# Performance work log

Hardware: AMD Instinct MI355X
Metric: run time of the kernel (lower is better)

The kernel has to match this reference:

```python
import jax, jax.numpy as jnp
import numpy as np

VOCAB, EMBED, HIDDEN = 50000, 256, 512
B, SEQ = 64, 200


def setup_inputs() -> dict:
    key = jax.random.key(0)
    ks = jax.random.split(key, 16)
    h2 = 2 * HIDDEN
    inp = {
        "input_idx": jax.random.randint(ks[0], (B,), 0, VOCAB),
        "encoded": jax.random.normal(ks[1], (B, SEQ, h2), jnp.float32),
        "encoded_idx": jax.random.randint(ks[2], (B, SEQ), 0, VOCAB),
        "prev_state": jax.random.normal(ks[3], (B, HIDDEN), jnp.float32),
        "weighted": jax.random.normal(ks[4], (B, 1, h2), jnp.float32),
        "order": 1,
        # learned parameters
        "embed_table": jax.random.normal(ks[5], (VOCAB, EMBED), jnp.float32) * 0.02,
        "w_ih": jax.random.normal(ks[6], (3 * HIDDEN, EMBED + h2), jnp.float32) * 0.02,
        "w_hh": jax.random.normal(ks[7], (3 * HIDDEN, HIDDEN), jnp.float32) * 0.02,
        "b_ih": jax.random.normal(ks[8], (3 * HIDDEN,), jnp.float32) * 0.02,
        "b_hh": jax.random.normal(ks[9], (3 * HIDDEN,), jnp.float32) * 0.02,
        "wo_w": jax.random.normal(ks[10], (VOCAB, HIDDEN), jnp.float32) * 0.02,
        "wo_b": jax.random.normal(ks[11], (VOCAB,), jnp.float32) * 0.02,
        "wc_w": jax.random.normal(ks[12], (HIDDEN, h2), jnp.float32) * 0.02,
        "wc_b": jax.random.normal(ks[13], (HIDDEN,), jnp.float32) * 0.02,
    }
    return inp


def _gru_step(x, h, w_ih, w_hh, b_ih, b_hh):
    # torch GRU gate ordering: reset, update, new
    gx = x @ w_ih.T + b_ih            # [b, 3h]
    gh = h @ w_hh.T + b_hh            # [b, 3h]
    xr, xz, xn = jnp.split(gx, 3, axis=-1)
    hr, hz, hn = jnp.split(gh, 3, axis=-1)
    r = jax.nn.sigmoid(xr + hr)
    z = jax.nn.sigmoid(xz + hz)
    n = jnp.tanh(xn + r * hn)
    return (1.0 - z) * n + z * h


def reference(input_idx, encoded, encoded_idx, prev_state, weighted, order,
              embed_table, w_ih, w_hh, b_ih, b_hh, wo_w, wo_b, wc_w, wc_b):
    b, seq, _ = encoded.shape
    vocab = wo_w.shape[0]

    # GRU single step on [embed(input); weighted]
    x = jnp.concatenate([embed_table[input_idx], weighted[:, 0, :]], axis=-1)
    state = _gru_step(x, prev_state, w_ih, w_hh, b_ih, b_hh)  # [b, h]

    # generate score over vocab
    score_g = state @ wo_w.T + wo_b                           # [b, vocab]

    # copy score over source positions
    score_c = jnp.tanh(jnp.einsum('bsk,hk->bsh', encoded, wc_w) + wc_b)
    score_c = jnp.einsum('bsh,bh->bs', score_c, state)        # [b, seq]

    encoded_mask = (encoded_idx != 0).astype(score_c.dtype)
    idx_from_input = (encoded_idx == input_idx[:, None]).astype(score_c.dtype)
    score_c = score_c * encoded_mask * idx_from_input

    # joint softmax over [vocab + seq]
    probs = jax.nn.softmax(jnp.concatenate([score_g, score_c], axis=1), axis=1)
    prob_g = probs[:, :vocab]
    prob_c = probs[:, vocab:]                                 # [b, seq]

    # scatter copy probs into vocab space (equivalent to one-hot bmm)
    flat_idx = (jnp.arange(b)[:, None] * vocab + encoded_idx).reshape(-1)
    prob_c_to_g = jnp.zeros((b * vocab,), probs.dtype).at[flat_idx].add(
        prob_c.reshape(-1)).reshape(b, vocab)

    out = (prob_g + prob_c_to_g)[:, None, :]                  # [b, 1, vocab]

    # selective-read attention, renormalized where sum > 0 (detached divisor)
    attn = prob_c * idx_from_input
    s = jax.lax.stop_gradient(jnp.sum(attn, axis=1, keepdims=True))
    attn = jnp.where(s > 0.0, attn / jnp.where(s > 0.0, s, 1.0), attn)
    weighted_new = jnp.einsum('bs,bsk->bk', attn, encoded)[:, None, :]  # [b,1,2h]

    return out, state, weighted_new
```

## Files before the change

kernel.cpp:

```cpp
#include <hip/hip_runtime.h>
#include <hip/hip_bf16.h>
#include <cstdint>
#include <cstddef>

#define VOCAB  50000
#define EMBED  256
#define HIDDEN 512
#define BATCH  64
#define SEQ    200
#define H2     1024
#define XDIM   1280
#define G3     1536
#define V4     (VOCAB/4)
#define NVB    782
#define NVBP   784
#define NFB    13

typedef __attribute__((ext_vector_type(8))) short short8;
typedef __attribute__((ext_vector_type(4))) float f32x4;

__device__ __forceinline__ short f2bf(float f) {
  uint32_t u = __builtin_bit_cast(uint32_t, f);
  uint32_t r = (u + 0x7fffu + ((u >> 16) & 1u)) >> 16;
  return (short)(r & 0xffffu);
}

__device__ __forceinline__ short8 pack8(float4 v0, float4 v1) {
  short8 fr;
  fr[0]=f2bf(v0.x); fr[1]=f2bf(v0.y); fr[2]=f2bf(v0.z); fr[3]=f2bf(v0.w);
  fr[4]=f2bf(v1.x); fr[5]=f2bf(v1.y); fr[6]=f2bf(v1.z); fr[7]=f2bf(v1.w);
  return fr;
}

__launch_bounds__(256)
__global__ void gru_gemm(const int* __restrict__ idx, const float* __restrict__ embed,
                         const float* __restrict__ weighted, const float* __restrict__ h0,
                         const float* __restrict__ w_ih, const float* __restrict__ w_hh,
                         float* __restrict__ gxp, float* __restrict__ ghp) {
  __shared__ __align__(16) short As[4 * 64 * 8];
  const int tid  = threadIdx.x;
  const int wave = tid >> 6, lane = tid & 63;
  const int l15  = lane & 15, lk = lane >> 4;
  const int slice = blockIdx.y;
  const bool isX  = slice < 8;
  const float* B  = isX ? w_ih : w_hh;
  const int ldb   = isX ? XDIM : HIDDEN;
  const int kbeg  = isX ? slice * 160 : (slice - 8) * 128;
  const int kend  = kbeg + (isX ? 160 : 128);
  float* C = isX ? (gxp + (size_t)slice * BATCH * G3)
                 : (ghp + (size_t)(slice - 8) * BATCH * G3);
  const int ncol = blockIdx.x * 64 + wave * 16;

  f32x4 acc0 = {0,0,0,0}, acc1 = {0,0,0,0}, acc2 = {0,0,0,0}, acc3 = {0,0,0,0};

  const int sl  = tid & 63;
  const int sm  = (tid >> 6) * 16 + (sl & 15);
  const int skb = (sl >> 4) * 8;

  const int nrow = ncol + l15;
  const float* Bbase = B + (size_t)nrow * ldb + lk * 8;

  for (int kc = kbeg; kc < kend; kc += 32) {
    {
      const float4* ap;
      if (isX) {
        int col = kc + skb;
        if (col < EMBED) ap = reinterpret_cast<const float4*>(embed + (size_t)idx[sm] * EMBED + col);
        else             ap = reinterpret_cast<const float4*>(weighted + (size_t)sm * H2 + (col - EMBED));
      } else {
        ap = reinterpret_cast<const float4*>(h0 + (size_t)sm * HIDDEN + kc + skb);
      }
      *reinterpret_cast<short8*>(&As[tid * 8]) = pack8(ap[0], ap[1]);
    }
    __syncthreads();
    short8 bf;
    {
      const float4* bp = reinterpret_cast<const float4*>(Bbase + kc);
      bf = pack8(bp[0], bp[1]);
    }
    short8 a0 = *reinterpret_cast<const short8*>(&As[(0*64 + lane)*8]);
    short8 a1 = *reinterpret_cast<const short8*>(&As[(1*64 + lane)*8]);
    short8 a2 = *reinterpret_cast<const short8*>(&As[(2*64 + lane)*8]);
    short8 a3 = *reinterpret_cast<const short8*>(&As[(3*64 + lane)*8]);
    acc0 = __builtin_amdgcn_mfma_f32_16x16x32_bf16(a0, bf, acc0, 0, 0, 0);
    acc1 = __builtin_amdgcn_mfma_f32_16x16x32_bf16(a1, bf, acc1, 0, 0, 0);
    acc2 = __builtin_amdgcn_mfma_f32_16x16x32_bf16(a2, bf, acc2, 0, 0, 0);
    acc3 = __builtin_amdgcn_mfma_f32_16x16x32_bf16(a3, bf, acc3, 0, 0, 0);
    __syncthreads();
  }

  const int n = ncol + l15;
  #pragma unroll
  for (int r = 0; r < 4; ++r) {
    C[(size_t)(0*16 + lk*4 + r) * G3 + n] = acc0[r];
    C[(size_t)(1*16 + lk*4 + r) * G3 + n] = acc1[r];
    C[(size_t)(2*16 + lk*4 + r) * G3 + n] = acc2[r];
    C[(size_t)(3*16 + lk*4 + r) * G3 + n] = acc3[r];
  }
}

__launch_bounds__(256)
__global__ void gru_gates(const float* __restrict__ gxp, const float* __restrict__ ghp,
                          const float* __restrict__ b_ih, const float* __restrict__ b_hh,
                          const float* __restrict__ h0, float* __restrict__ out_state,
                          unsigned short* __restrict__ stateF) {
  int i = blockIdx.x * 256 + threadIdx.x;
  int b = i >> 9, h = i & 511;
  float xr = b_ih[h], xz = b_ih[HIDDEN + h], xn = b_ih[2*HIDDEN + h];
  #pragma unroll
  for (int s = 0; s < 8; ++s) {
    const float* g = gxp + (size_t)s * BATCH * G3 + (size_t)b * G3;
    xr += g[h]; xz += g[HIDDEN + h]; xn += g[2*HIDDEN + h];
  }
  float hr = b_hh[h], hz = b_hh[HIDDEN + h], hn = b_hh[2*HIDDEN + h];
  #pragma unroll
  for (int s = 0; s < 4; ++s) {
    const float* g = ghp + (size_t)s * BATCH * G3 + (size_t)b * G3;
    hr += g[h]; hz += g[HIDDEN + h]; hn += g[2*HIDDEN + h];
  }
  float r = 1.f / (1.f + __expf(-(xr + hr)));
  float z = 1.f / (1.f + __expf(-(xz + hz)));
  float n = tanhf(xn + r * hn);
  float st = (1.f - z) * n + z * h0[(size_t)b*HIDDEN + h];
  out_state[(size_t)b*HIDDEN + h] = st;
  int fi = ((h >> 5) * 4 + (b >> 4)) * 512 + ((b & 15) + 16 * ((h >> 3) & 3)) * 8 + (h & 7);
  stateF[fi] = (unsigned short)f2bf(st);
}

__launch_bounds__(256)
__global__ void vocab_fused(const unsigned short* __restrict__ stateF,
                            const float* __restrict__ state,
                            const float* __restrict__ wo_w, const float* __restrict__ wo_b,
                            const int* __restrict__ eidx, const int* __restrict__ iidx,
                            const float* __restrict__ enc, const float* __restrict__ wc_w,
                            const float* __restrict__ wc_b,
                            float* __restrict__ E, float* __restrict__ escc,
                            float* __restrict__ Spart) {
  __shared__ float red[256];
  __shared__ float sval[SEQ];
  __shared__ int   act[SEQ];
  const int bid = blockIdx.x;
  const int tid = threadIdx.x;

  if (bid < BATCH) {
    const int b = bid;
    const int in0 = iidx[b];
    if (tid < SEQ) {
      int e = eidx[b*SEQ + tid];
      act[tid]  = (e != 0 && e == in0);
      sval[tid] = 0.f;
    }
    __syncthreads();
    for (int sq = 0; sq < SEQ; ++sq) {
      if (act[sq]) {
        const float4* er = reinterpret_cast<const float4*>(enc + (size_t)b*SEQ*H2 + (size_t)sq*H2);
        float part_sum = 0.f;
        for (int h = tid; h < HIDDEN; h += 256) {
          const float4* wr = reinterpret_cast<const float4*>(wc_w + (size_t)h*H2);
          float d = wc_b[h];
          for (int k = 0; k < H2/4; ++k) {
            float4 a = er[k], w = wr[k];
            d += a.x*w.x + a.y*w.y + a.z*w.z + a.w*w.w;
          }
          part_sum += tanhf(d) * state[(size_t)b*HIDDEN + h];
        }
        red[tid] = part_sum;
        __syncthreads();
        for (int off = 128; off > 0; off >>= 1) {
          if (tid < off) red[tid] += red[tid + off];
          __syncthreads();
        }
        if (tid == 0) sval[sq] = red[0];
        __syncthreads();
      }
    }
    __syncthreads();
    float ex = 0.f;
    if (tid < SEQ) {
      ex = __expf(sval[tid]);
      escc[b*SEQ + tid] = ex;
    }
    red[tid] = ex;
    __syncthreads();
    for (int off = 128; off > 0; off >>= 1) {
      if (tid < off) red[tid] += red[tid + off];
      __syncthreads();
    }
    if (tid == 0) Spart[(size_t)b * NVBP + NVB] = red[0];
    return;
  }

  const int vb   = bid - BATCH;
  const int wave = tid >> 6, lane = tid & 63;
  const int l15  = lane & 15, lk = lane >> 4;
  const int ncol = vb * 64 + wave * 16;
  int nrow = ncol + l15; if (nrow > VOCAB - 1) nrow = VOCAB - 1;
  const float*  Bb = wo_w + (size_t)nrow * HIDDEN + lk * 8;
  const short8* Af = reinterpret_cast<const short8*>(stateF);

  f32x4 acc0 = {0,0,0,0}, acc1 = {0,0,0,0}, acc2 = {0,0,0,0}, acc3 = {0,0,0,0};
  #pragma unroll 4
  for (int c = 0; c < 16; ++c) {
    const float4* bp = reinterpret_cast<const float4*>(Bb + c*32);
    float4 b0 = bp[0], b1 = bp[1];
    short8 a0 = Af[(c*4 + 0)*64 + lane];
    short8 a1 = Af[(c*4 + 1)*64 + lane];
    short8 a2 = Af[(c*4 + 2)*64 + lane];
    short8 a3 = Af[(c*4 + 3)*64 + lane];
    short8 bf = pack8(b0, b1);
    acc0 = __builtin_amdgcn_mfma_f32_16x16x32_bf16(a0, bf, acc0, 0, 0, 0);
    acc1 = __builtin_amdgcn_mfma_f32_16x16x32_bf16(a1, bf, acc1, 0, 0, 0);
    acc2 = __builtin_amdgcn_mfma_f32_16x16x32_bf16(a2, bf, acc2, 0, 0, 0);
    acc3 = __builtin_amdgcn_mfma_f32_16x16x32_bf16(a3, bf, acc3, 0, 0, 0);
  }

  const int n = ncol + l15;
  const bool valid = n < VOCAB;
  const float bv = valid ? wo_b[n] : 0.f;
  f32x4 accs[4] = {acc0, acc1, acc2, acc3};
  #pragma unroll
  for (int a = 0; a < 4; ++a) {
    #pragma unroll
    for (int r = 0; r < 4; ++r) {
      float ev = valid ? __expf(accs[a][r] + bv) : 0.f;
      if (valid) E[(size_t)(a*16 + lk*4 + r) * VOCAB + n] = ev;
      float v = ev;
      v += __shfl_xor(v, 1); v += __shfl_xor(v, 2);
      v += __shfl_xor(v, 4); v += __shfl_xor(v, 8);
      if (l15 == 0) red[wave*64 + a*16 + lk*4 + r] = v;
    }
  }
  __syncthreads();
  if (tid < 64)
    Spart[(size_t)tid * NVBP + vb] =
        red[0*64+tid] + red[1*64+tid] + red[2*64+tid] + red[3*64+tid];
}

__launch_bounds__(256)
__global__ void finalize_fused(const int* __restrict__ eidx, const int* __restrict__ iidx,
                               const float* __restrict__ escc, const float* __restrict__ Spart,
                               const float* __restrict__ enc,
                               float* __restrict__ out0, float* __restrict__ wnew) {
  const int bid = blockIdx.x;
  const int tid = threadIdx.x;

  if (bid < BATCH) {
    __shared__ float attn_sh[SEQ];
    __shared__ float fnorm_sh;
    const int b = bid;
    const int in0 = iidx[b];
    if (tid < SEQ) {
      int e = eidx[b*SEQ + tid];
      attn_sh[tid] = (e == in0) ? escc[b*SEQ + tid] : 0.f;
    }
    __syncthreads();
    if (tid == 0) {
      float s = 0.f;
      for (int i = 0; i < SEQ; ++i) s += attn_sh[i];
      fnorm_sh = (s > 0.f) ? 1.f / s : 1.f;
    }
    __syncthreads();
    const float f = fnorm_sh;
    float a0 = 0, a1 = 0, a2 = 0, a3 = 0;
    const float4* ep = reinterpret_cast<const float4*>(enc + (size_t)b*SEQ*H2);
    for (int s = 0; s < SEQ; ++s) {
      float a = attn_sh[s];
      if (a != 0.f) {
        a *= f;
        float4 v = ep[(size_t)s*(H2/4) + tid];
        a0 += a*v.x; a1 += a*v.y; a2 += a*v.z; a3 += a*v.w;
      }
    }
    float4 o = {a0, a1, a2, a3};
    reinterpret_cast<float4*>(wnew + (size_t)b*H2)[tid] = o;
    return;
  }

  __shared__ int   me[SEQ];
  __shared__ float mp[SEQ];
  __shared__ float sred[256];
  __shared__ int   cnt;
  const int q = bid - BATCH;
  const int b = q / NFB, c = q % NFB;
  if (tid == 0) cnt = 0;
  float ps = 0.f;
  for (int i = tid; i < NVB + 1; i += 256) ps += Spart[(size_t)b * NVBP + i];
  sred[tid] = ps;
  __syncthreads();
  if (tid < SEQ) {
    int e = eidx[b*SEQ + tid];
    if ((unsigned)(e - c*4096) < 4096u) {
      int j = atomicAdd(&cnt, 1);
      me[j] = e; mp[j] = escc[b*SEQ + tid];
    }
  }
  for (int off = 128; off > 0; off >>= 1) {
    __syncthreads();
    if (tid < off) sred[tid] += sred[tid + off];
  }
  __syncthreads();
  const float inv = 1.f / sred[0];
  const int ncnt = cnt;
  #pragma unroll
  for (int t = 0; t < 4; ++t) {
    const int i4 = c * 1024 + t * 256 + tid;
    if (i4 < V4) {
      float4 v = reinterpret_cast<const float4*>(out0 + (size_t)b*VOCAB)[i4];
      float4 o;
      o.x = v.x * inv; o.y = v.y * inv; o.z = v.z * inv; o.w = v.w * inv;
      const int base = i4 * 4;
      for (int j = 0; j < ncnt; ++j) {
        unsigned d = (unsigned)(me[j] - base);
        if (d < 4u) (&o.x)[d] += mp[j] * inv;
      }
      reinterpret_cast<float4*>(out0 + (size_t)b*VOCAB)[i4] = o;
    }
  }
}

extern "C" void kernel_launch(void* const* d_in, const int* in_sizes, int n_in,
                              void* d_out, int out_size, void* d_ws, size_t ws_size,
                              hipStream_t stream) {
  (void)in_sizes; (void)n_in; (void)out_size; (void)ws_size;
  const int*   input_idx  = (const int*)d_in[0];
  const float* encoded    = (const float*)d_in[1];
  const int*   enc_idx    = (const int*)d_in[2];
  const float* prev_state = (const float*)d_in[3];
  const float* weighted   = (const float*)d_in[4];
  const float* embed      = (const float*)d_in[6];
  const float* w_ih       = (const float*)d_in[7];
  const float* w_hh       = (const float*)d_in[8];
  const float* b_ih       = (const float*)d_in[9];
  const float* b_hh       = (const float*)d_in[10];
  const float* wo_w       = (const float*)d_in[11];
  const float* wo_b       = (const float*)d_in[12];
  const float* wc_w       = (const float*)d_in[13];
  const float* wc_b       = (const float*)d_in[14];

  float* out0      = (float*)d_out;
  float* out_state = out0 + (size_t)BATCH * VOCAB;
  float* out_wnew  = out_state + BATCH * HIDDEN;

  float* ws    = (float*)d_ws;
  float* gxp   = ws;
  float* ghp   = ws + (size_t)8 * BATCH * G3;
  unsigned short* stateF = (unsigned short*)(ws + (size_t)12 * BATCH * G3);
  float* escc  = ws + (size_t)12 * BATCH * G3 + 16384;
  float* Spart = escc + BATCH * SEQ;

  gru_gemm<<<dim3(G3/64, 12), 256, 0, stream>>>(input_idx, embed, weighted, prev_state,
                                                w_ih, w_hh, gxp, ghp);
  gru_gates<<<(BATCH*HIDDEN)/256, 256, 0, stream>>>(gxp, ghp, b_ih, b_hh, prev_state,
                                                    out_state, stateF);
  vocab_fused<<<BATCH + NVB, 256, 0, stream>>>(stateF, out_state, wo_w, wo_b,
                                               enc_idx, input_idx, encoded, wc_w, wc_b,
                                               out0, escc, Spart);
  finalize_fused<<<BATCH + BATCH*NFB, 256, 0, stream>>>(enc_idx, input_idx, escc, Spart,
                                                        encoded, out0, out_wnew);
}
```

Measured before the change: 83.16 us.

## Fuse vocab GEMM and finalize into one cooperative kernel with grid syncs

Merges the vocab projection kernel and the finalize kernel into a single cooperative launch. The exp'd logits stay in registers across grid-wide barriers and are normalized and scattered in place, instead of being written to the output and re-read in a second pass. Each vocab block rescans all encoded indices to build its own copy-scatter list in shared memory. The MFMA loop is also software-pipelined with a one-step prefetch. In exchange it pays for two grid syncs, the redundant index scans, and a fixed MCAP limit on the scatter list.

```diff
diff --git a/kernel.cpp b/kernel.cpp
--- a/kernel.cpp
+++ b/kernel.cpp
@@ -1,7 +1,10 @@
 #include <hip/hip_runtime.h>
+#include <hip/hip_cooperative_groups.h>
 #include <hip/hip_bf16.h>
 #include <cstdint>
 #include <cstddef>
+
+namespace cg = cooperative_groups;
 
 #define VOCAB  50000
 #define EMBED  256
@@ -14,7 +17,7 @@
 #define V4     (VOCAB/4)
 #define NVB    782
 #define NVBP   784
-#define NFB    13
+#define MCAP   2048
 
 typedef __attribute__((ext_vector_type(8))) short short8;
 typedef __attribute__((ext_vector_type(4))) float f32x4;
@@ -127,18 +130,24 @@
   stateF[fi] = (unsigned short)f2bf(st);
 }
 
-__launch_bounds__(256)
-__global__ void vocab_fused(const unsigned short* __restrict__ stateF,
-                            const float* __restrict__ state,
-                            const float* __restrict__ wo_w, const float* __restrict__ wo_b,
-                            const int* __restrict__ eidx, const int* __restrict__ iidx,
-                            const float* __restrict__ enc, const float* __restrict__ wc_w,
-                            const float* __restrict__ wc_b,
-                            float* __restrict__ E, float* __restrict__ escc,
-                            float* __restrict__ Spart) {
+__launch_bounds__(256, 4)
+__global__ void vocab_coop(const unsigned short* __restrict__ stateF,
+                           const float* __restrict__ state,
+                           const float* __restrict__ wo_w, const float* __restrict__ wo_b,
+                           const int* __restrict__ eidx, const int* __restrict__ iidx,
+                           const float* __restrict__ enc, const float* __restrict__ wc_w,
+                           const float* __restrict__ wc_b,
+                           float* __restrict__ out0, float* __restrict__ wnew,
+                           float* __restrict__ escc, float* __restrict__ Spart,
+                           float* __restrict__ Svec) {
+  cg::grid_group grid = cg::this_grid();
   __shared__ float red[256];
   __shared__ float sval[SEQ];
   __shared__ int   act[SEQ];
+  __shared__ int   me[MCAP];
+  __shared__ float mprob[MCAP];
+  __shared__ float Ssh[BATCH];
+  __shared__ int   mcnt;
   const int bid = blockIdx.x;
   const int tid = threadIdx.x;
 
@@ -187,6 +196,45 @@
       __syncthreads();
     }
     if (tid == 0) Spart[(size_t)b * NVBP + NVB] = red[0];
+    __threadfence();
+    grid.sync();
+
+    float ps = 0.f;
+    for (int i = tid; i < NVB + 1; i += 256) ps += Spart[(size_t)b * NVBP + i];
+    red[tid] = ps;
+    __syncthreads();
+    for (int off = 128; off > 0; off >>= 1) {
+      if (tid < off) red[tid] += red[tid + off];
+      __syncthreads();
+    }
+    if (tid == 0) Svec[b] = red[0];
+
+    {
+      float attn = 0.f;
+      float fsum = 0.f;
+      if (tid == 0) {
+        float s = 0.f;
+        for (int i = 0; i < SEQ; ++i)
+          if (act[i]) s += __expf(sval[i]);
+        red[0] = (s > 0.f) ? 1.f / s : 1.f;
+      }
+      __syncthreads();
+      const float f = red[0];
+      (void)attn; (void)fsum;
+      float a0 = 0, a1 = 0, a2 = 0, a3 = 0;
+      const float4* ep = reinterpret_cast<const float4*>(enc + (size_t)b*SEQ*H2);
+      for (int s = 0; s < SEQ; ++s) {
+        if (act[s]) {
+          float a = __expf(sval[s]) * f;
+          float4 v = ep[(size_t)s*(H2/4) + tid];
+          a0 += a*v.x; a1 += a*v.y; a2 += a*v.z; a3 += a*v.w;
+        }
+      }
+      float4 o = {a0, a1, a2, a3};
+      reinterpret_cast<float4*>(wnew + (size_t)b*H2)[tid] = o;
+    }
+    __threadfence();
+    grid.sync();
     return;
   }
 
@@ -198,122 +246,119 @@
   const float*  Bb = wo_w + (size_t)nrow * HIDDEN + lk * 8;
   const short8* Af = reinterpret_cast<const short8*>(stateF);
 
+  if (tid == 0) mcnt = 0;
+
   f32x4 acc0 = {0,0,0,0}, acc1 = {0,0,0,0}, acc2 = {0,0,0,0}, acc3 = {0,0,0,0};
-  #pragma unroll 4
-  for (int c = 0; c < 16; ++c) {
-    const float4* bp = reinterpret_cast<const float4*>(Bb + c*32);
-    float4 b0 = bp[0], b1 = bp[1];
-    short8 a0 = Af[(c*4 + 0)*64 + lane];
-    short8 a1 = Af[(c*4 + 1)*64 + lane];
-    short8 a2 = Af[(c*4 + 2)*64 + lane];
-    short8 a3 = Af[(c*4 + 3)*64 + lane];
-    short8 bf = pack8(b0, b1);
-    acc0 = __builtin_amdgcn_mfma_f32_16x16x32_bf16(a0, bf, acc0, 0, 0, 0);
-    acc1 = __builtin_amdgcn_mfma_f32_16x16x32_bf16(a1, bf, acc1, 0, 0, 0);
-    acc2 = __builtin_amdgcn_mfma_f32_16x16x32_bf16(a2, bf, acc2, 0, 0, 0);
-    acc3 = __builtin_amdgcn_mfma_f32_16x16x32_bf16(a3, bf, acc3, 0, 0, 0);
+  {
+    const float4* bp0 = reinterpret_cast<const float4*>(Bb);
+    float4 b0 = bp0[0], b1 = bp0[1];
+    short8 a0 = Af[0*64 + lane], a1 = Af[1*64 + lane];
+    short8 a2 = Af[2*64 + lane], a3 = Af[3*64 + lane];
+    #pragma unroll
+    for (int c = 0; c < 16; ++c) {
+      float4 nb0, nb1; short8 n0, n1, n2, n3;
+      if (c < 15) {
+        const float4* bp = reinterpret_cast<const float4*>(Bb + (c+1)*32);
+        nb0 = bp[0]; nb1 = bp[1];
+        n0 = Af[((c+1)*4 + 0)*64 + lane];
+        n1 = Af[((c+1)*4 + 1)*64 + lane];
+        n2 = Af[((c+1)*4 + 2)*64 + lane];
+        n3 = Af[((c+1)*4 + 3)*64 + lane];
+      }
+      short8 bf = pack8(b0, b1);
+      acc0 = __builtin_amdgcn_mfma_f32_16x16x32_bf16(a0, bf, acc0, 0, 0, 0);
+      acc1 = __builtin_amdgcn_mfma_f32_16x16x32_bf16(a1, bf, acc1, 0, 0, 0);
+      acc2 = __builtin_amdgcn_mfma_f32_16x16x32_bf16(a2, bf, acc2, 0, 0, 0);
+      acc3 = __builtin_amdgcn_mfma_f32_16x16x32_bf16(a3, bf, acc3, 0, 0, 0);
+      if (c < 15) { b0 = nb0; b1 = nb1; a0 = n0; a1 = n1; a2 = n2; a3 = n3; }
+    }
   }
 
   const int n = ncol + l15;
   const bool valid = n < VOCAB;
   const float bv = valid ? wo_b[n] : 0.f;
-  f32x4 accs[4] = {acc0, acc1, acc2, acc3};
-  #pragma unroll
-  for (int a = 0; a < 4; ++a) {
-    #pragma unroll
-    for (int r = 0; r < 4; ++r) {
-      float ev = valid ? __expf(accs[a][r] + bv) : 0.f;
-      if (valid) E[(size_t)(a*16 + lk*4 + r) * VOCAB + n] = ev;
-      float v = ev;
-      v += __shfl_xor(v, 1); v += __shfl_xor(v, 2);
-      v += __shfl_xor(v, 4); v += __shfl_xor(v, 8);
-      if (l15 == 0) red[wave*64 + a*16 + lk*4 + r] = v;
+  #pragma unroll
+  for (int r = 0; r < 4; ++r) {
+    acc0[r] = valid ? __expf(acc0[r] + bv) : 0.f;
+    acc1[r] = valid ? __expf(acc1[r] + bv) : 0.f;
+    acc2[r] = valid ? __expf(acc2[r] + bv) : 0.f;
+    acc3[r] = valid ? __expf(acc3[r] + bv) : 0.f;
+  }
+  #pragma unroll
+  for (int r = 0; r < 4; ++r) {
+    float v0 = acc0[r], v1 = acc1[r], v2 = acc2[r], v3 = acc3[r];
+    v0 += __shfl_xor(v0,1); v0 += __shfl_xor(v0,2); v0 += __shfl_xor(v0,4); v0 += __shfl_xor(v0,8);
+    v1 += __shfl_xor(v1,1); v1 += __shfl_xor(v1,2); v1 += __shfl_xor(v1,4); v1 += __shfl_xor(v1,8);
+    v2 += __shfl_xor(v2,1); v2 += __shfl_xor(v2,2); v2 += __shfl_xor(v2,4); v2 += __shfl_xor(v2,8);
+    v3 += __shfl_xor(v3,1); v3 += __shfl_xor(v3,2); v3 += __shfl_xor(v3,4); v3 += __shfl_xor(v3,8);
+    if (l15 == 0) {
+      red[wave*64 + 0*16 + lk*4 + r] = v0;
+      red[wave*64 + 1*16 + lk*4 + r] = v1;
+      red[wave*64 + 2*16 + lk*4 + r] = v2;
+      red[wave*64 + 3*16 + lk*4 + r] = v3;
     }
   }
   __syncthreads();
   if (tid < 64)
     Spart[(size_t)tid * NVBP + vb] =
         red[0*64+tid] + red[1*64+tid] + red[2*64+tid] + red[3*64+tid];
-}
-
-__launch_bounds__(256)
-__global__ void finalize_fused(const int* __restrict__ eidx, const int* __restrict__ iidx,
-                               const float* __restrict__ escc, const float* __restrict__ Spart,
-                               const float* __restrict__ enc,
-                               float* __restrict__ out0, float* __restrict__ wnew) {
-  const int bid = blockIdx.x;
-  const int tid = threadIdx.x;
-
-  if (bid < BATCH) {
-    __shared__ float attn_sh[SEQ];
-    __shared__ float fnorm_sh;
-    const int b = bid;
-    const int in0 = iidx[b];
-    if (tid < SEQ) {
-      int e = eidx[b*SEQ + tid];
-      attn_sh[tid] = (e == in0) ? escc[b*SEQ + tid] : 0.f;
-    }
-    __syncthreads();
-    if (tid == 0) {
-      float s = 0.f;
-      for (int i = 0; i < SEQ; ++i) s += attn_sh[i];
-      fnorm_sh = (s > 0.f) ? 1.f / s : 1.f;
-    }
-    __syncthreads();
-    const float f = fnorm_sh;
-    float a0 = 0, a1 = 0, a2 = 0, a3 = 0;
-    const float4* ep = reinterpret_cast<const float4*>(enc + (size_t)b*SEQ*H2);
-    for (int s = 0; s < SEQ; ++s) {
-      float a = attn_sh[s];
-      if (a != 0.f) {
-        a *= f;
-        float4 v = ep[(size_t)s*(H2/4) + tid];
-        a0 += a*v.x; a1 += a*v.y; a2 += a*v.z; a3 += a*v.w;
-      }
-    }
-    float4 o = {a0, a1, a2, a3};
-    reinterpret_cast<float4*>(wnew + (size_t)b*H2)[tid] = o;
-    return;
-  }
-
-  __shared__ int   me[SEQ];
-  __shared__ float mp[SEQ];
-  __shared__ float sred[256];
-  __shared__ int   cnt;
-  const int q = bid - BATCH;
-  const int b = q / NFB, c = q % NFB;
-  if (tid == 0) cnt = 0;
-  float ps = 0.f;
-  for (int i = tid; i < NVB + 1; i += 256) ps += Spart[(size_t)b * NVBP + i];
-  sred[tid] = ps;
+
+  const int colLo = vb * 64;
+  for (int j = tid; j < BATCH*SEQ; j += 256) {
+    int e = eidx[j];
+    if ((unsigned)(e - colLo) < 64u) {
+      int k = atomicAdd(&mcnt, 1);
+      if (k < MCAP) me[k] = (j << 16) | e;
+    }
+  }
   __syncthreads();
-  if (tid < SEQ) {
-    int e = eidx[b*SEQ + tid];
-    if ((unsigned)(e - c*4096) < 4096u) {
-      int j = atomicAdd(&cnt, 1);
-      me[j] = e; mp[j] = escc[b*SEQ + tid];
-    }
-  }
-  for (int off = 128; off > 0; off >>= 1) {
-    __syncthreads();
-    if (tid < off) sred[tid] += sred[tid + off];
-  }
+  __threadfence();
+  grid.sync();
+  grid.sync();
+
+  if (tid < BATCH) Ssh[tid] = Svec[tid];
+  int nc = mcnt; if (nc > MCAP) nc = MCAP;
   __syncthreads();
-  const float inv = 1.f / sred[0];
-  const int ncnt = cnt;
-  #pragma unroll
-  for (int t = 0; t < 4; ++t) {
-    const int i4 = c * 1024 + t * 256 + tid;
-    if (i4 < V4) {
-      float4 v = reinterpret_cast<const float4*>(out0 + (size_t)b*VOCAB)[i4];
-      float4 o;
-      o.x = v.x * inv; o.y = v.y * inv; o.z = v.z * inv; o.w = v.w * inv;
-      const int base = i4 * 4;
-      for (int j = 0; j < ncnt; ++j) {
-        unsigned d = (unsigned)(me[j] - base);
-        if (d < 4u) (&o.x)[d] += mp[j] * inv;
-      }
-      reinterpret_cast<float4*>(out0 + (size_t)b*VOCAB)[i4] = o;
+  for (int k = tid; k < nc; k += 256) {
+    int j = me[k] >> 16;
+    int b = j / SEQ, s = j - b * SEQ;
+    mprob[k] = escc[b*SEQ + s] / Ssh[b];
+  }
+  __syncthreads();
+
+  #pragma unroll
+  for (int r = 0; r < 4; ++r) {
+    acc0[r] *= 1.f / Ssh[0*16 + lk*4 + r];
+    acc1[r] *= 1.f / Ssh[1*16 + lk*4 + r];
+    acc2[r] *= 1.f / Ssh[2*16 + lk*4 + r];
+    acc3[r] *= 1.f / Ssh[3*16 + lk*4 + r];
+  }
+
+  for (int k = 0; k < nc; ++k) {
+    const int pk = me[k];
+    const int e  = pk & 0xffff;
+    const int j  = pk >> 16;
+    const int b  = j / SEQ;
+    const bool laneHit = (((e - colLo) >> 4) == wave) && ((e & 15) == l15)
+                         && (((b >> 2) & 3) == lk);
+    const float add = laneHit ? mprob[k] : 0.f;
+    const int ba = b >> 4, br = b & 3;
+    #pragma unroll
+    for (int r = 0; r < 4; ++r) {
+      acc0[r] += (ba == 0 && br == r) ? add : 0.f;
+      acc1[r] += (ba == 1 && br == r) ? add : 0.f;
+      acc2[r] += (ba == 2 && br == r) ? add : 0.f;
+      acc3[r] += (ba == 3 && br == r) ? add : 0.f;
+    }
+  }
+
+  if (valid) {
+    #pragma unroll
+    for (int r = 0; r < 4; ++r) {
+      out0[(size_t)(0*16 + lk*4 + r) * VOCAB + n] = acc0[r];
+      out0[(size_t)(1*16 + lk*4 + r) * VOCAB + n] = acc1[r];
+      out0[(size_t)(2*16 + lk*4 + r) * VOCAB + n] = acc2[r];
+      out0[(size_t)(3*16 + lk*4 + r) * VOCAB + n] = acc3[r];
     }
   }
 }
@@ -347,14 +392,20 @@
   unsigned short* stateF = (unsigned short*)(ws + (size_t)12 * BATCH * G3);
   float* escc  = ws + (size_t)12 * BATCH * G3 + 16384;
   float* Spart = escc + BATCH * SEQ;
+  float* Svec  = Spart + (size_t)BATCH * NVBP;
 
   gru_gemm<<<dim3(G3/64, 12), 256, 0, stream>>>(input_idx, embed, weighted, prev_state,
                                                 w_ih, w_hh, gxp, ghp);
   gru_gates<<<(BATCH*HIDDEN)/256, 256, 0, stream>>>(gxp, ghp, b_ih, b_hh, prev_state,
                                                     out_state, stateF);
-  vocab_fused<<<BATCH + NVB, 256, 0, stream>>>(stateF, out_state, wo_w, wo_b,
-                                               enc_idx, input_idx, encoded, wc_w, wc_b,
-                                               out0, escc, Spart);
-  finalize_fused<<<BATCH + BATCH*NFB, 256, 0, stream>>>(enc_idx, input_idx, escc, Spart,
-                                                        encoded, out0, out_wnew);
-}
+
+  const unsigned short* stateF_c = stateF;
+  const float* state_c = out_state;
+  void* kargs[] = {
+    (void*)&stateF_c, (void*)&state_c, (void*)&wo_w, (void*)&wo_b,
+    (void*)&enc_idx, (void*)&input_idx, (void*)&encoded, (void*)&wc_w, (void*)&wc_b,
+    (void*)&out0, (void*)&out_wnew, (void*)&escc, (void*)&Spart, (void*)&Svec
+  };
+  hipLaunchCooperativeKernel((const void*)vocab_coop, dim3(BATCH + NVB), dim3(256),
+                             kargs, 0, stream);
+}
```

Result: slower. 268.5 us (+222.9%).

## Stage wo_w tiles through swizzled per-wave LDS double buffer in vocab GEMM

Applied to the files above, without the earlier changes.

The vocab projection kernel no longer feeds each MFMA lane 8 floats of wo_w straight from global memory. Each wave now loads 128-column chunks of its 16 rows with wider contiguous row reads, converts them to bf16, and writes them into an XOR-swizzled per-wave LDS double buffer. MFMA B fragments are then read back from LDS. The aim is better coalescing of the dominant wo_w stream, at the cost of 32KB of extra LDS per block (lower occupancy) and extra LDS read/write traffic. The buffer reuse relies on in-wave ordering with no explicit barrier.

```diff
diff --git a/kernel.cpp b/kernel.cpp
--- a/kernel.cpp
+++ b/kernel.cpp
@@ -17,6 +17,7 @@
 #define NFB    13
 
 typedef __attribute__((ext_vector_type(8))) short short8;
+typedef __attribute__((ext_vector_type(4))) short short4v;
 typedef __attribute__((ext_vector_type(4))) float f32x4;
 
 __device__ __forceinline__ short f2bf(float f) {
@@ -128,17 +129,18 @@
 }
 
 __launch_bounds__(256)
-__global__ void vocab_fused(const unsigned short* __restrict__ stateF,
-                            const float* __restrict__ state,
-                            const float* __restrict__ wo_w, const float* __restrict__ wo_b,
-                            const int* __restrict__ eidx, const int* __restrict__ iidx,
-                            const float* __restrict__ enc, const float* __restrict__ wc_w,
-                            const float* __restrict__ wc_b,
-                            float* __restrict__ E, float* __restrict__ escc,
-                            float* __restrict__ Spart) {
+__global__ void vocab_v3(const unsigned short* __restrict__ stateF,
+                         const float* __restrict__ state,
+                         const float* __restrict__ wo_w, const float* __restrict__ wo_b,
+                         const int* __restrict__ eidx, const int* __restrict__ iidx,
+                         const float* __restrict__ enc, const float* __restrict__ wc_w,
+                         const float* __restrict__ wc_b,
+                         float* __restrict__ E, float* __restrict__ escc,
+                         float* __restrict__ Spart) {
   __shared__ float red[256];
   __shared__ float sval[SEQ];
   __shared__ int   act[SEQ];
+  __shared__ __align__(16) unsigned short Bst[4][2][2048];
   const int bid = blockIdx.x;
   const int tid = threadIdx.x;
 
@@ -194,24 +196,51 @@
   const int wave = tid >> 6, lane = tid & 63;
   const int l15  = lane & 15, lk = lane >> 4;
   const int ncol = vb * 64 + wave * 16;
-  int nrow = ncol + l15; if (nrow > VOCAB - 1) nrow = VOCAB - 1;
-  const float*  Bb = wo_w + (size_t)nrow * HIDDEN + lk * 8;
   const short8* Af = reinterpret_cast<const short8*>(stateF);
+  unsigned short* Bw = &Bst[wave][0][0];
 
   f32x4 acc0 = {0,0,0,0}, acc1 = {0,0,0,0}, acc2 = {0,0,0,0}, acc3 = {0,0,0,0};
-  #pragma unroll 4
-  for (int c = 0; c < 16; ++c) {
-    const float4* bp = reinterpret_cast<const float4*>(Bb + c*32);
-    float4 b0 = bp[0], b1 = bp[1];
-    short8 a0 = Af[(c*4 + 0)*64 + lane];
-    short8 a1 = Af[(c*4 + 1)*64 + lane];
-    short8 a2 = Af[(c*4 + 2)*64 + lane];
-    short8 a3 = Af[(c*4 + 3)*64 + lane];
-    short8 bf = pack8(b0, b1);
-    acc0 = __builtin_amdgcn_mfma_f32_16x16x32_bf16(a0, bf, acc0, 0, 0, 0);
-    acc1 = __builtin_amdgcn_mfma_f32_16x16x32_bf16(a1, bf, acc1, 0, 0, 0);
-    acc2 = __builtin_amdgcn_mfma_f32_16x16x32_bf16(a2, bf, acc2, 0, 0, 0);
-    acc3 = __builtin_amdgcn_mfma_f32_16x16x32_bf16(a3, bf, acc3, 0, 0, 0);
+
+  const int srow  = 2 * 0 + (lane >> 5);
+  const int scol4 = (lane & 31) * 4;
+
+  auto STAGE = [&](int sc) {
+    unsigned short* dst = Bw + (sc & 1) * 2048;
+    #pragma unroll
+    for (int j = 0; j < 8; ++j) {
+      int r = 2*j + (lane >> 5);
+      int grow = ncol + r; if (grow > VOCAB - 1) grow = VOCAB - 1;
+      float4 v = *reinterpret_cast<const float4*>(wo_w + (size_t)grow * HIDDEN + sc*128 + scol4);
+      short4v s4; s4[0]=f2bf(v.x); s4[1]=f2bf(v.y); s4[2]=f2bf(v.z); s4[3]=f2bf(v.w);
+      int uo = scol4 ^ ((r & 7) << 3);
+      *reinterpret_cast<short4v*>(dst + r*128 + uo) = s4;
+    }
+  };
+  (void)srow;
+
+  auto COMPUTE = [&](int sc) {
+    const unsigned short* src = Bw + (sc & 1) * 2048;
+    #pragma unroll
+    for (int g = 0; g < 4; ++g) {
+      const int c = sc*4 + g;
+      const int uo = (g*32 + lk*8) ^ ((l15 & 7) << 3);
+      short8 bf = *reinterpret_cast<const short8*>(src + l15*128 + uo);
+      short8 a0 = Af[(c*4 + 0)*64 + lane];
+      short8 a1 = Af[(c*4 + 1)*64 + lane];
+      short8 a2 = Af[(c*4 + 2)*64 + lane];
+      short8 a3 = Af[(c*4 + 3)*64 + lane];
+      acc0 = __builtin_amdgcn_mfma_f32_16x16x32_bf16(a0, bf, acc0, 0, 0, 0);
+      acc1 = __builtin_amdgcn_mfma_f32_16x16x32_bf16(a1, bf, acc1, 0, 0, 0);
+      acc2 = __builtin_amdgcn_mfma_f32_16x16x32_bf16(a2, bf, acc2, 0, 0, 0);
+      acc3 = __builtin_amdgcn_mfma_f32_16x16x32_bf16(a3, bf, acc3, 0, 0, 0);
+    }
+  };
+
+  STAGE(0);
+  #pragma unroll
+  for (int sc = 0; sc < 4; ++sc) {
+    if (sc < 3) STAGE(sc + 1);
+    COMPUTE(sc);
   }
 
   const int n = ncol + l15;
@@ -352,9 +381,9 @@
                                                 w_ih, w_hh, gxp, ghp);
   gru_gates<<<(BATCH*HIDDEN)/256, 256, 0, stream>>>(gxp, ghp, b_ih, b_hh, prev_state,
                                                     out_state, stateF);
-  vocab_fused<<<BATCH + NVB, 256, 0, stream>>>(stateF, out_state, wo_w, wo_b,
-                                               enc_idx, input_idx, encoded, wc_w, wc_b,
-                                               out0, escc, Spart);
+  vocab_v3<<<BATCH + NVB, 256, 0, stream>>>(stateF, out_state, wo_w, wo_b,
+                                            enc_idx, input_idx, encoded, wc_w, wc_b,
+                                            out0, escc, Spart);
   finalize_fused<<<BATCH + BATCH*NFB, 256, 0, stream>>>(enc_idx, input_idx, escc, Spart,
                                                         encoded, out0, out_wnew);
 }
```

New measurement: 80.89 us. 2.7% less time.

## Split copy-score computation across hidden slices and defer exp/sum to finalize

Applied to the files above, without the earlier changes.

The copy-score branch previously used one block per batch row, with each thread running a 1024-long dot product over its hidden units. It now uses 8 blocks per batch row, each covering 64 hidden units, with 4 threads splitting every dot product and combining through shuffles. The per-slice partial scores go to a workspace array, and the exp and the softmax denominator move into the finalize kernel, which adds up the 8 partials. This shortens the serial tail of the vocab kernel, at the cost of extra blocks and a small amount of repeated partial-sum work in every finalize block.

```diff
diff --git a/kernel.cpp b/kernel.cpp
--- a/kernel.cpp
+++ b/kernel.cpp
@@ -15,6 +15,8 @@
 #define NVB    782
 #define NVBP   784
 #define NFB    13
+#define NHS    8
+#define NSCC   (BATCH*NHS)
 
 typedef __attribute__((ext_vector_type(8))) short short8;
 typedef __attribute__((ext_vector_type(4))) float f32x4;
@@ -128,69 +130,59 @@
 }
 
 __launch_bounds__(256)
-__global__ void vocab_fused(const unsigned short* __restrict__ stateF,
-                            const float* __restrict__ state,
-                            const float* __restrict__ wo_w, const float* __restrict__ wo_b,
-                            const int* __restrict__ eidx, const int* __restrict__ iidx,
-                            const float* __restrict__ enc, const float* __restrict__ wc_w,
-                            const float* __restrict__ wc_b,
-                            float* __restrict__ E, float* __restrict__ escc,
-                            float* __restrict__ Spart) {
+__global__ void vocab_v5(const unsigned short* __restrict__ stateF,
+                         const float* __restrict__ state,
+                         const float* __restrict__ wo_w, const float* __restrict__ wo_b,
+                         const int* __restrict__ eidx, const int* __restrict__ iidx,
+                         const float* __restrict__ enc, const float* __restrict__ wc_w,
+                         const float* __restrict__ wc_b,
+                         float* __restrict__ E, float* __restrict__ sccp,
+                         float* __restrict__ Spart) {
   __shared__ float red[256];
-  __shared__ float sval[SEQ];
   __shared__ int   act[SEQ];
   const int bid = blockIdx.x;
   const int tid = threadIdx.x;
 
-  if (bid < BATCH) {
-    const int b = bid;
+  if (bid < NSCC) {
+    const int b  = bid >> 3, hs = bid & 7;
     const int in0 = iidx[b];
     if (tid < SEQ) {
       int e = eidx[b*SEQ + tid];
-      act[tid]  = (e != 0 && e == in0);
-      sval[tid] = 0.f;
-    }
-    __syncthreads();
+      act[tid] = (e != 0 && e == in0);
+      sccp[(size_t)(b*SEQ + tid)*NHS + hs] = 0.f;
+    }
+    __syncthreads();
+    const int hl = tid >> 2, kq = tid & 3;
+    const int h  = hs*64 + hl;
+    const float4* wr = reinterpret_cast<const float4*>(wc_w + (size_t)h*H2) + kq*64;
+    const float  sh  = state[(size_t)b*HIDDEN + h];
+    const float  bh  = wc_b[h];
     for (int sq = 0; sq < SEQ; ++sq) {
       if (act[sq]) {
-        const float4* er = reinterpret_cast<const float4*>(enc + (size_t)b*SEQ*H2 + (size_t)sq*H2);
-        float part_sum = 0.f;
-        for (int h = tid; h < HIDDEN; h += 256) {
-          const float4* wr = reinterpret_cast<const float4*>(wc_w + (size_t)h*H2);
-          float d = wc_b[h];
-          for (int k = 0; k < H2/4; ++k) {
-            float4 a = er[k], w = wr[k];
-            d += a.x*w.x + a.y*w.y + a.z*w.z + a.w*w.w;
-          }
-          part_sum += tanhf(d) * state[(size_t)b*HIDDEN + h];
+        const float4* er = reinterpret_cast<const float4*>(enc + (size_t)b*SEQ*H2 + (size_t)sq*H2) + kq*64;
+        float d = 0.f;
+        #pragma unroll 8
+        for (int k = 0; k < 64; ++k) {
+          float4 a = er[k], w = wr[k];
+          d += a.x*w.x + a.y*w.y + a.z*w.z + a.w*w.w;
         }
-        red[tid] = part_sum;
+        d += __shfl_xor(d, 1);
+        d += __shfl_xor(d, 2);
+        float ph = (kq == 0) ? tanhf(d + bh) * sh : 0.f;
+        red[tid] = ph;
         __syncthreads();
         for (int off = 128; off > 0; off >>= 1) {
           if (tid < off) red[tid] += red[tid + off];
           __syncthreads();
         }
-        if (tid == 0) sval[sq] = red[0];
+        if (tid == 0) sccp[(size_t)(b*SEQ + sq)*NHS + hs] = red[0];
         __syncthreads();
       }
     }
-    __syncthreads();
-    float ex = 0.f;
-    if (tid < SEQ) {
-      ex = __expf(sval[tid]);
-      escc[b*SEQ + tid] = ex;
-    }
-    red[tid] = ex;
-    __syncthreads();
-    for (int off = 128; off > 0; off >>= 1) {
-      if (tid < off) red[tid] += red[tid + off];
-      __syncthreads();
-    }
-    if (tid == 0) Spart[(size_t)b * NVBP + NVB] = red[0];
     return;
   }
 
-  const int vb   = bid - BATCH;
+  const int vb   = bid - NSCC;
   const int wave = tid >> 6, lane = tid & 63;
   const int l15  = lane & 15, lk = lane >> 4;
   const int ncol = vb * 64 + wave * 16;
@@ -238,7 +230,7 @@
 
 __launch_bounds__(256)
 __global__ void finalize_fused(const int* __restrict__ eidx, const int* __restrict__ iidx,
-                               const float* __restrict__ escc, const float* __restrict__ Spart,
+                               const float* __restrict__ sccp, const float* __restrict__ Spart,
                                const float* __restrict__ enc,
                                float* __restrict__ out0, float* __restrict__ wnew) {
   const int bid = blockIdx.x;
@@ -250,8 +242,11 @@
     const int b = bid;
     const int in0 = iidx[b];
     if (tid < SEQ) {
+      float sc = 0.f;
+      #pragma unroll
+      for (int hs = 0; hs < NHS; ++hs) sc += sccp[(size_t)(b*SEQ + tid)*NHS + hs];
       int e = eidx[b*SEQ + tid];
-      attn_sh[tid] = (e == in0) ? escc[b*SEQ + tid] : 0.f;
+      attn_sh[tid] = (e == in0) ? __expf(sc) : 0.f;
     }
     __syncthreads();
     if (tid == 0) {
@@ -284,15 +279,21 @@
   const int b = q / NFB, c = q % NFB;
   if (tid == 0) cnt = 0;
   float ps = 0.f;
-  for (int i = tid; i < NVB + 1; i += 256) ps += Spart[(size_t)b * NVBP + i];
-  sred[tid] = ps;
+  for (int i = tid; i < NVB; i += 256) ps += Spart[(size_t)b * NVBP + i];
+  float ex = 0.f;
+  int e = -1;
+  if (tid < SEQ) {
+    float sc = 0.f;
+    #pragma unroll
+    for (int hs = 0; hs < NHS; ++hs) sc += sccp[(size_t)(b*SEQ + tid)*NHS + hs];
+    ex = __expf(sc);
+    e = eidx[b*SEQ + tid];
+  }
+  sred[tid] = ps + ex;
   __syncthreads();
-  if (tid < SEQ) {
-    int e = eidx[b*SEQ + tid];
-    if ((unsigned)(e - c*4096) < 4096u) {
-      int j = atomicAdd(&cnt, 1);
-      me[j] = e; mp[j] = escc[b*SEQ + tid];
-    }
+  if (tid < SEQ && (unsigned)(e - c*4096) < 4096u) {
+    int j = atomicAdd(&cnt, 1);
+    me[j] = e; mp[j] = ex;
   }
   for (int off = 128; off > 0; off >>= 1) {
     __syncthreads();
@@ -345,16 +346,16 @@
   float* gxp   = ws;
   float* ghp   = ws + (size_t)8 * BATCH * G3;
   unsigned short* stateF = (unsigned short*)(ws + (size_t)12 * BATCH * G3);
-  float* escc  = ws + (size_t)12 * BATCH * G3 + 16384;
-  float* Spart = escc + BATCH * SEQ;
+  float* sccp  = ws + (size_t)12 * BATCH * G3 + 8192;
+  float* Spart = sccp + (size_t)BATCH * SEQ * NHS;
 
   gru_gemm<<<dim3(G3/64, 12), 256, 0, stream>>>(input_idx, embed, weighted, prev_state,
                                                 w_ih, w_hh, gxp, ghp);
   gru_gates<<<(BATCH*HIDDEN)/256, 256, 0, stream>>>(gxp, ghp, b_ih, b_hh, prev_state,
                                                     out_state, stateF);
-  vocab_fused<<<BATCH + NVB, 256, 0, stream>>>(stateF, out_state, wo_w, wo_b,
-                                               enc_idx, input_idx, encoded, wc_w, wc_b,
-                                               out0, escc, Spart);
-  finalize_fused<<<BATCH + BATCH*NFB, 256, 0, stream>>>(enc_idx, input_idx, escc, Spart,
+  vocab_v5<<<NSCC + NVB, 256, 0, stream>>>(stateF, out_state, wo_w, wo_b,
+                                           enc_idx, input_idx, encoded, wc_w, wc_b,
+                                           out0, sccp, Spart);
+  finalize_fused<<<BATCH + BATCH*NFB, 256, 0, stream>>>(enc_idx, input_idx, sccp, Spart,
                                                         encoded, out0, out_wnew);
 }
```

Measured after the change: 82.29 us. No clear change (-1.0%).
